# Performance work log

Hardware: AMD Instinct MI355X
Metric: run time of the kernel (lower is better)

The kernel has to match this reference:

```python
import jax, jax.numpy as jnp
import numpy as np

B, T, D, W, H = 8, 2048, 1024, 16, 8
HD = D // H  # head dim = 128
EPS = 1e-5


def _layernorm(x, g, b):
    m = jnp.mean(x, axis=-1, keepdims=True)
    v = jnp.var(x, axis=-1, keepdims=True)
    return (x - m) / jnp.sqrt(v + EPS) * g + b


def setup_inputs() -> dict:
    key = jax.random.key(0)
    ks = jax.random.split(key, 8)
    s = 0.02
    return {
        "frame_features": jax.random.normal(ks[0], (B, T, D), dtype=jnp.float32),
        "frame_indices": jnp.arange(B * T, dtype=jnp.int64).reshape(B, T),
        # nn.MultiheadAttention packed in-projection (3D, D) and out projection
        "w_qkv": jax.random.normal(ks[1], (3 * D, D), dtype=jnp.float32) * s,
        "b_qkv": jnp.zeros((3 * D,), dtype=jnp.float32),
        "w_out": jax.random.normal(ks[2], (D, D), dtype=jnp.float32) * s,
        "b_out": jnp.zeros((D,), dtype=jnp.float32),
        # FFN: Linear(D, 4D) -> GELU -> Linear(4D, D)
        "w1": jax.random.normal(ks[3], (4 * D, D), dtype=jnp.float32) * s,
        "b1": jnp.zeros((4 * D,), dtype=jnp.float32),
        "w2": jax.random.normal(ks[4], (D, 4 * D), dtype=jnp.float32) * s,
        "b2": jnp.zeros((D,), dtype=jnp.float32),
        "g1": jnp.ones((D,), dtype=jnp.float32),
        "beta1": jnp.zeros((D,), dtype=jnp.float32),
        "g2": jnp.ones((D,), dtype=jnp.float32),
        "beta2": jnp.zeros((D,), dtype=jnp.float32),
    }


def _forward(frame_features, frame_indices, w_qkv, b_qkv, w_out, b_out,
             w1, b1, w2, b2, g1, beta1, g2, beta2):
    # --- sinusoidal temporal positional encoding, indexed by frame number ---
    pos = frame_indices.astype(jnp.float32)[..., None]          # (B, T, 1)
    div = jnp.exp(-jnp.log(10000.0) * jnp.arange(0, D, 2, dtype=jnp.float32) / D)
    ang = pos * div                                              # (B, T, D/2)
    pe = jnp.stack([jnp.sin(ang), jnp.cos(ang)], axis=-1).reshape(B, T, D)
    x = frame_features + pe

    # --- block-diagonal (local window) attention, all windows in one pass ---
    nw = T // W
    xw = x.reshape(B, nw, W, D)
    qkv = jnp.einsum('bnwd,ed->bnwe', xw, w_qkv) + b_qkv         # (B, nw, W, 3D)
    q, k, v = jnp.split(qkv, 3, axis=-1)
    q = q.reshape(B, nw, W, H, HD)
    k = k.reshape(B, nw, W, H, HD)
    v = v.reshape(B, nw, W, H, HD)
    scores = jnp.einsum('bnqhd,bnkhd->bnhqk', q, k) / jnp.sqrt(jnp.float32(HD))
    attn = jax.nn.softmax(scores, axis=-1)
    o = jnp.einsum('bnhqk,bnkhd->bnqhd', attn, v).reshape(B, nw, W, D)
    attn_out = jnp.einsum('bnwd,ed->bnwe', o, w_out) + b_out

    h = _layernorm(xw + attn_out, g1, beta1)
    ffn = jnp.einsum('bnwf,df->bnwd', jax.nn.gelu(
        jnp.einsum('bnwd,fd->bnwf', h, w1) + b1, approximate=False), w2) + b2
    out = _layernorm(h + ffn, g2, beta2)
    return out.reshape(B, T, D)


def reference(frame_features, frame_indices, w_qkv, b_qkv, w_out, b_out,
              w1, b1, w2, b2, g1, beta1, g2, beta2):
    return _forward(frame_features, frame_indices, w_qkv, b_qkv, w_out, b_out,
                    w1, b1, w2, b2, g1, beta1, g2, beta2)
```

## Files before the change

### kernel.cpp

```cpp
#include <hip/hip_runtime.h>
#include <math.h>

typedef __bf16 bf16;
typedef __bf16 bf16x8 __attribute__((ext_vector_type(8)));
typedef __bf16 bf16x4 __attribute__((ext_vector_type(4)));
typedef __bf16 bf16x2 __attribute__((ext_vector_type(2)));
typedef float f32x4 __attribute__((ext_vector_type(4)));

#define ROWS 16384

typedef __attribute__((address_space(3))) void* lds_vp;
typedef const __attribute__((address_space(1))) void* glb_vp;
__device__ __forceinline__ void gload16(const void* g, void* l) {
  __builtin_amdgcn_global_load_lds((glb_vp)g, (lds_vp)l, 16, 0, 0);
}

__global__ __launch_bounds__(256) void cast_kernel(
    const float* __restrict__ src, bf16* __restrict__ dst, int n)
{
  int i = (blockIdx.x * 256 + threadIdx.x) * 8;
  if (i >= n) return;
  float4 a = *(const float4*)(src + i);
  float4 b = *(const float4*)(src + i + 4);
  bf16x8 o;
  o[0] = (bf16)a.x; o[1] = (bf16)a.y; o[2] = (bf16)a.z; o[3] = (bf16)a.w;
  o[4] = (bf16)b.x; o[5] = (bf16)b.y; o[6] = (bf16)b.z; o[7] = (bf16)b.w;
  *(bf16x8*)(dst + i) = o;
}

__global__ __launch_bounds__(256) void pe_add_kernel(
    const float* __restrict__ ff, const int* __restrict__ idx, bf16* __restrict__ x)
{
  int p   = blockIdx.x * 256 + threadIdx.x;
  int row = p >> 9;
  int j   = p & 511;
  float pos = (float)idx[row];
  float d2  = (float)(2 * j) * (1.0f / 1024.0f);
  float dv  = expf(-9.210340371976184f * d2);
  float ang = pos * dv;
  float s, c;
  sincosf(ang, &s, &c);
  int base = row * 1024 + 2 * j;
  float2 f = *(const float2*)(ff + base);
  bf16x2 o;
  o[0] = (bf16)(f.x + s);
  o[1] = (bf16)(f.y + c);
  *(bf16x2*)(x + base) = o;
}

#define MFMA16 __builtin_amdgcn_mfma_f32_16x16x32_bf16

template<bool GELU, bool RES>
__global__ __launch_bounds__(512, 2) void gemm8(
    const bf16* __restrict__ A, const bf16* __restrict__ Bw,
    const float* __restrict__ bias, const bf16* __restrict__ resid,
    bf16* __restrict__ C, int M, int N, int K)
{
  extern __shared__ char smem[];
  bf16* lA = (bf16*)smem;
  bf16* lB = (bf16*)(smem + 65536);

  const int tid  = threadIdx.x;
  const int wave = tid >> 6;
  const int lane = tid & 63;
  const int wm = wave >> 2, wn = wave & 3;
  const int ln = lane & 15, q = lane >> 4;
  const int wm8 = wm * 8, wn4 = wn * 4;
  const int rsw = (ln * 32 + q * 8) ^ (((ln >> 3) & 1) << 4);

  const int nwg = gridDim.x;
  const int nbn = N >> 8;
  const int swz = (blockIdx.x & 7) * (nwg >> 3) + (blockIdx.x >> 3);
  const int bm = (swz / nbn) << 8;
  const int bn = (swz % nbn) << 8;

  const int le = lane ^ (((lane >> 5) & 1) << 1);
  const int sr = le >> 2;
  const int sc = (le & 3) * 8;
  const bf16* gA = A  + (size_t)(bm + wave * 16 + sr) * K + sc;
  const bf16* gB = Bw + (size_t)(bn + wave * 16 + sr) * K + sc;
  const size_t hstep = (size_t)128 * K;

#define STAGE_A(h, bb, kk) do { \
    bf16* _d = lA + (bb) * 16384 + ((h) * 8 + wave) * 1024; \
    gload16(gA + (size_t)(h) * hstep + (kk), _d); \
    gload16(gA + (size_t)(h) * hstep + (kk) + 32, _d + 512); } while (0)
#define STAGE_B(h, bb, kk) do { \
    bf16* _d = lB + (bb) * 16384 + ((h) * 8 + wave) * 1024; \
    gload16(gB + (size_t)(h) * hstep + (kk), _d); \
    gload16(gB + (size_t)(h) * hstep + (kk) + 32, _d + 512); } while (0)
#define LDA8(dst, t, ks, bb) (dst) = *(const bf16x8*)(lA + (bb) * 16384 + (wm8 + (t)) * 1024 + (ks) * 512 + rsw)
#define LDB8(dst, n, ks, bb) (dst) = *(const bf16x8*)(lB + (bb) * 16384 + (wn4 + (n)) * 1024 + (ks) * 512 + rsw)

  f32x4 acc[8][4];
#pragma unroll
  for (int i = 0; i < 8; i++)
#pragma unroll
    for (int j = 0; j < 4; j++) acc[i][j] = {0.f, 0.f, 0.f, 0.f};

  const int nkt = K >> 6;

  STAGE_A(0, 0, 0);  STAGE_A(1, 0, 0);
  STAGE_B(0, 0, 0);  STAGE_B(1, 0, 0);
  STAGE_A(0, 1, 64); STAGE_A(1, 1, 64);
  asm volatile("s_waitcnt vmcnt(4)");

  bf16x8 alo[4][2], ahi[4][2], bq[2][2];

  for (int m = 0; m < nkt; ++m) {
    const int b  = m & 1;
    const int k0 = m << 6;

    __builtin_amdgcn_s_barrier();
    if (m + 1 < nkt) STAGE_B(0, b ^ 1, k0 + 64);
#pragma unroll
    for (int t = 0; t < 4; t++) { LDA8(alo[t][0], t, 0, b); LDA8(alo[t][1], t, 1, b); }
    LDB8(bq[0][0], 0, 0, b); LDB8(bq[0][1], 0, 1, b);
    LDB8(bq[1][0], 1, 0, b); LDB8(bq[1][1], 1, 1, b);
    __builtin_amdgcn_s_setprio(1);
#pragma unroll
    for (int t = 0; t < 4; t++)
#pragma unroll
      for (int n = 0; n < 2; n++) {
        acc[t][n] = MFMA16(alo[t][0], bq[n][0], acc[t][n], 0, 0, 0);
        acc[t][n] = MFMA16(alo[t][1], bq[n][1], acc[t][n], 0, 0, 0);
      }
    __builtin_amdgcn_s_setprio(0);

    __builtin_amdgcn_s_barrier();
    if (m + 1 < nkt) STAGE_B(1, b ^ 1, k0 + 64);
#pragma unroll
    for (int t = 0; t < 4; t++) { LDA8(ahi[t][0], t + 4, 0, b); LDA8(ahi[t][1], t + 4, 1, b); }
    __builtin_amdgcn_s_setprio(1);
#pragma unroll
    for (int t = 0; t < 4; t++)
#pragma unroll
      for (int n = 0; n < 2; n++) {
        acc[t + 4][n] = MFMA16(ahi[t][0], bq[n][0], acc[t + 4][n], 0, 0, 0);
        acc[t + 4][n] = MFMA16(ahi[t][1], bq[n][1], acc[t + 4][n], 0, 0, 0);
      }
    __builtin_amdgcn_s_setprio(0);

    __builtin_amdgcn_s_barrier();
    if (m + 2 < nkt) STAGE_A(0, b, k0 + 128);
    LDB8(bq[0][0], 2, 0, b); LDB8(bq[0][1], 2, 1, b);
    LDB8(bq[1][0], 3, 0, b); LDB8(bq[1][1], 3, 1, b);
    __builtin_amdgcn_s_setprio(1);
#pragma unroll
    for (int t = 0; t < 4; t++)
#pragma unroll
      for (int n = 0; n < 2; n++) {
        acc[t][n + 2] = MFMA16(alo[t][0], bq[n][0], acc[t][n + 2], 0, 0, 0);
        acc[t][n + 2] = MFMA16(alo[t][1], bq[n][1], acc[t][n + 2], 0, 0, 0);
      }
    __builtin_amdgcn_s_setprio(0);

    __builtin_amdgcn_s_barrier();
    if (m + 2 < nkt) STAGE_A(1, b, k0 + 128);
    __builtin_amdgcn_s_setprio(1);
#pragma unroll
    for (int t = 0; t < 4; t++)
#pragma unroll
      for (int n = 0; n < 2; n++) {
        acc[t + 4][n + 2] = MFMA16(ahi[t][0], bq[n][0], acc[t + 4][n + 2], 0, 0, 0);
        acc[t + 4][n + 2] = MFMA16(ahi[t][1], bq[n][1], acc[t + 4][n + 2], 0, 0, 0);
      }
    __builtin_amdgcn_s_setprio(0);
    if (m == nkt - 2)     { asm volatile("s_waitcnt vmcnt(0)"); }
    else if (m < nkt - 2) { asm volatile("s_waitcnt vmcnt(4)"); }
  }

  float bv[4];
#pragma unroll
  for (int tn = 0; tn < 4; tn++) bv[tn] = bias[bn + wn * 64 + tn * 16 + ln];
  bf16* eb = (bf16*)smem;
  const int lrow = tid >> 4;
  const int cb   = (tid & 15) * 16;
#pragma unroll
  for (int tm = 0; tm < 8; tm++) {
    __syncthreads();
#pragma unroll
    for (int tn = 0; tn < 4; tn++)
#pragma unroll
      for (int i = 0; i < 4; i++)
        eb[(wm * 16 + q * 4 + i) * 264 + wn * 64 + tn * 16 + ln] =
            (bf16)(acc[tm][tn][i] + bv[tn]);
    __syncthreads();
    int gR = bm + (lrow >> 4) * 128 + tm * 16 + (lrow & 15);
    size_t rowoff = (size_t)gR * N + bn + cb;
    bf16x8 v0 = *(const bf16x8*)&eb[lrow * 264 + cb];
    bf16x8 v1 = *(const bf16x8*)&eb[lrow * 264 + cb + 8];
    if (RES) {
      bf16x8 r0 = *(const bf16x8*)(resid + rowoff);
      bf16x8 r1 = *(const bf16x8*)(resid + rowoff + 8);
#pragma unroll
      for (int u = 0; u < 8; u++) {
        v0[u] = (bf16)((float)v0[u] + (float)r0[u]);
        v1[u] = (bf16)((float)v1[u] + (float)r1[u]);
      }
    }
    if (GELU) {
#pragma unroll
      for (int u = 0; u < 8; u++) {
        float a = (float)v0[u], c = (float)v1[u];
        float ea = __builtin_amdgcn_exp2f(2.3022082f * a * (1.0f + 0.044715f * a * a));
        float ec = __builtin_amdgcn_exp2f(2.3022082f * c * (1.0f + 0.044715f * c * c));
        v0[u] = (bf16)(a - a * __builtin_amdgcn_rcpf(ea + 1.0f));
        v1[u] = (bf16)(c - c * __builtin_amdgcn_rcpf(ec + 1.0f));
      }
    }
    *(bf16x8*)(C + rowoff)     = v0;
    *(bf16x8*)(C + rowoff + 8) = v1;
  }
#undef STAGE_A
#undef STAGE_B
#undef LDA8
#undef LDB8
}

__global__ __launch_bounds__(256) void attn_kernel(
    const bf16* __restrict__ qkv, bf16* __restrict__ o)
{
  __shared__ float sq[16][132], sk[16][132], sv[16][132];
  __shared__ float ss[16][17];

  int wid = blockIdx.x;
  int h   = wid & 7;
  int win = wid >> 3;
  int tb  = win * 16;

  int t  = threadIdx.x;
  int r  = t >> 4;
  int c8 = (t & 15) * 8;

  const bf16* base = qkv + (size_t)(tb + r) * 3072 + c8;
  bf16x8 qv = *(const bf16x8*)(base + h * 128);
  bf16x8 kv = *(const bf16x8*)(base + 1024 + h * 128);
  bf16x8 vv = *(const bf16x8*)(base + 2048 + h * 128);
#pragma unroll
  for (int u = 0; u < 8; u++) {
    sq[r][c8 + u] = (float)qv[u];
    sk[r][c8 + u] = (float)kv[u];
    sv[r][c8 + u] = (float)vv[u];
  }
  __syncthreads();

  {
    int i = t >> 4, jj = t & 15;
    float s = 0.f;
#pragma unroll 8
    for (int d = 0; d < 128; d++) s += sq[i][d] * sk[jj][d];
    ss[i][jj] = s * 0.08838834764831845f;
  }
  __syncthreads();

  if (t < 16) {
    float m = -1e30f;
    for (int jj = 0; jj < 16; jj++) m = fmaxf(m, ss[t][jj]);
    float sum = 0.f;
    for (int jj = 0; jj < 16; jj++) { float e = expf(ss[t][jj] - m); ss[t][jj] = e; sum += e; }
    float inv = 1.0f / sum;
    for (int jj = 0; jj < 16; jj++) ss[t][jj] *= inv;
  }
  __syncthreads();

  {
    int i = t >> 4; int d0 = (t & 15) * 8;
    float acc[8] = {0, 0, 0, 0, 0, 0, 0, 0};
#pragma unroll
    for (int jj = 0; jj < 16; jj++) {
      float a = ss[i][jj];
#pragma unroll
      for (int u = 0; u < 8; u++) acc[u] += a * sv[jj][d0 + u];
    }
    bf16* op = o + (size_t)(tb + i) * 1024 + h * 128 + d0;
#pragma unroll
    for (int u = 0; u < 8; u++) op[u] = (bf16)acc[u];
  }
}

template<typename OUT_T>
__global__ __launch_bounds__(256) void ln_kernel(
    const bf16* __restrict__ x, const float* __restrict__ g,
    const float* __restrict__ b, OUT_T* __restrict__ y)
{
  __shared__ float red[8];
  int row = blockIdx.x;
  int t   = threadIdx.x;
  int lane = t & 63, wave = t >> 6;

  bf16x4 v4 = *(const bf16x4*)(x + (size_t)row * 1024 + t * 4);
  float v[4];
  float s = 0.f, sq = 0.f;
#pragma unroll
  for (int u = 0; u < 4; u++) {
    v[u] = (float)v4[u];
    s += v[u];
    sq += v[u] * v[u];
  }
  for (int off = 32; off > 0; off >>= 1) {
    s  += __shfl_down(s, off);
    sq += __shfl_down(sq, off);
  }
  if (lane == 0) { red[wave * 2] = s; red[wave * 2 + 1] = sq; }
  __syncthreads();
  float st = red[0] + red[2] + red[4] + red[6];
  float qt = red[1] + red[3] + red[5] + red[7];
  float mean = st * (1.0f / 1024.0f);
  float var  = qt * (1.0f / 1024.0f) - mean * mean;
  float inv  = rsqrtf(var + 1e-5f);
  int c = t * 4;
  OUT_T* yr = y + (size_t)row * 1024 + c;
#pragma unroll
  for (int u = 0; u < 4; u++)
    yr[u] = (OUT_T)((v[u] - mean) * inv * g[c + u] + b[c + u]);
}

extern "C" void kernel_launch(void* const* d_in, const int* in_sizes, int n_in,
                              void* d_out, int out_size, void* d_ws, size_t ws_size,
                              hipStream_t stream) {
  const float* ff    = (const float*)d_in[0];
  const int*   idx   = (const int*)d_in[1];
  const float* w_qkv = (const float*)d_in[2];
  const float* b_qkv = (const float*)d_in[3];
  const float* w_out = (const float*)d_in[4];
  const float* b_out = (const float*)d_in[5];
  const float* w1    = (const float*)d_in[6];
  const float* b1    = (const float*)d_in[7];
  const float* w2    = (const float*)d_in[8];
  const float* b2    = (const float*)d_in[9];
  const float* g1    = (const float*)d_in[10];
  const float* be1   = (const float*)d_in[11];
  const float* g2    = (const float*)d_in[12];
  const float* be2   = (const float*)d_in[13];
  float* out = (float*)d_out;

  static bool attrs_done = false;
  if (!attrs_done) {
    attrs_done = true;
    hipFuncSetAttribute(reinterpret_cast<const void*>(&gemm8<false, false>),
                        hipFuncAttributeMaxDynamicSharedMemorySize, 131072);
    hipFuncSetAttribute(reinterpret_cast<const void*>(&gemm8<false, true>),
                        hipFuncAttributeMaxDynamicSharedMemorySize, 131072);
    hipFuncSetAttribute(reinterpret_cast<const void*>(&gemm8<true, false>),
                        hipFuncAttributeMaxDynamicSharedMemorySize, 131072);
  }

  char* p = (char*)d_ws;
  bf16* x_bf = (bf16*)p;  p += (size_t)ROWS * 1024 * 2;
  bf16* big  = (bf16*)p;  p += (size_t)ROWS * 4096 * 2;
  bf16* s_bf = (bf16*)p;  p += (size_t)ROWS * 1024 * 2;
  bf16* h_bf = (bf16*)p;  p += (size_t)ROWS * 1024 * 2;
  bf16* wqb  = (bf16*)p;  p += (size_t)3072 * 1024 * 2;
  bf16* wob  = (bf16*)p;  p += (size_t)1024 * 1024 * 2;
  bf16* w1b  = (bf16*)p;  p += (size_t)4096 * 1024 * 2;
  bf16* w2b  = (bf16*)p;  p += (size_t)1024 * 4096 * 2;
  bf16* o_bf = big + (size_t)ROWS * 3072;
  bf16* g_bf = big;

  cast_kernel<<<3072 * 1024 / 8 / 256, 256, 0, stream>>>(w_qkv, wqb, 3072 * 1024);
  cast_kernel<<<1024 * 1024 / 8 / 256, 256, 0, stream>>>(w_out, wob, 1024 * 1024);
  cast_kernel<<<4096 * 1024 / 8 / 256, 256, 0, stream>>>(w1, w1b, 4096 * 1024);
  cast_kernel<<<1024 * 4096 / 8 / 256, 256, 0, stream>>>(w2, w2b, 1024 * 4096);

  pe_add_kernel<<<ROWS * 512 / 256, 256, 0, stream>>>(ff, idx, x_bf);

  gemm8<false, false><<<64 * 12, 512, 131072, stream>>>(
      x_bf, wqb, b_qkv, nullptr, big, ROWS, 3072, 1024);
  attn_kernel<<<(ROWS / 16) * 8, 256, 0, stream>>>(big, o_bf);
  gemm8<false, true><<<64 * 4, 512, 131072, stream>>>(
      o_bf, wob, b_out, x_bf, s_bf, ROWS, 1024, 1024);
  ln_kernel<bf16><<<ROWS, 256, 0, stream>>>(s_bf, g1, be1, h_bf);
  gemm8<true, false><<<64 * 16, 512, 131072, stream>>>(
      h_bf, w1b, b1, nullptr, big, ROWS, 4096, 1024);
  gemm8<false, true><<<64 * 4, 512, 131072, stream>>>(
      g_bf, w2b, b2, h_bf, s_bf, ROWS, 1024, 4096);
  ln_kernel<float><<<ROWS, 256, 0, stream>>>(s_bf, g2, be2, out);
}
```

Measured before the change: 664.0 us.

## Rework GEMM mainloop into 4-stage K=32 pipeline with inline ds_read offsets

The bf16 GEMM main loop now uses K-steps of 32 with a four-buffer ring in LDS instead of a double-buffered K=64 scheme. Global-to-LDS loads are issued three stages ahead. LDS fragment reads use inline-asm ds_read_b128 with immediate offsets, and sched_barrier plus explicit lgkmcnt waits fence each MFMA burst. The goal is deeper prefetch to hide global latency and lower address-arithmetic overhead. The costs are more barriers per unit of K and a loop that assumes nkt is a multiple of 4 with a carefully tuned vmcnt sequence.

```diff
diff --git a/kernel.cpp b/kernel.cpp
--- a/kernel.cpp
+++ b/kernel.cpp
@@ -11,8 +11,16 @@
 
 typedef __attribute__((address_space(3))) void* lds_vp;
 typedef const __attribute__((address_space(1))) void* glb_vp;
+typedef __attribute__((address_space(3))) bf16 lbf16;
 __device__ __forceinline__ void gload16(const void* g, void* l) {
   __builtin_amdgcn_global_load_lds((glb_vp)g, (lds_vp)l, 16, 0, 0);
+}
+
+template<int OFF>
+__device__ __forceinline__ bf16x8 dsr(uint32_t a) {
+  bf16x8 r;
+  asm volatile("ds_read_b128 %0, %1 offset:%2" : "=v"(r) : "v"(a), "n"(OFF));
+  return r;
 }
 
 __global__ __launch_bounds__(256) void cast_kernel(
@@ -57,8 +65,6 @@
     bf16* __restrict__ C, int M, int N, int K)
 {
   extern __shared__ char smem[];
-  bf16* lA = (bf16*)smem;
-  bf16* lB = (bf16*)(smem + 65536);
 
   const int tid  = threadIdx.x;
   const int wave = tid >> 6;
@@ -66,7 +72,6 @@
   const int wm = wave >> 2, wn = wave & 3;
   const int ln = lane & 15, q = lane >> 4;
   const int wm8 = wm * 8, wn4 = wn * 4;
-  const int rsw = (ln * 32 + q * 8) ^ (((ln >> 3) & 1) << 4);
 
   const int nwg = gridDim.x;
   const int nbn = N >> 8;
@@ -74,23 +79,27 @@
   const int bm = (swz / nbn) << 8;
   const int bn = (swz % nbn) << 8;
 
+  const uint32_t lbase = (uint32_t)(size_t)(lbf16*)smem;
+  const uint32_t rswb  = (uint32_t)((ln * 64 + q * 16) ^ (((ln >> 3) & 1) << 5));
+  const uint32_t rA01 = lbase + wm8 * 1024 + rswb;
+  const uint32_t rA23 = rA01 + 65536;
+  const uint32_t rB01 = lbase + 16384 + wn4 * 1024 + rswb;
+  const uint32_t rB23 = rB01 + 65536;
+
   const int le = lane ^ (((lane >> 5) & 1) << 1);
   const int sr = le >> 2;
   const int sc = (le & 3) * 8;
-  const bf16* gA = A  + (size_t)(bm + wave * 16 + sr) * K + sc;
-  const bf16* gB = Bw + (size_t)(bn + wave * 16 + sr) * K + sc;
-  const size_t hstep = (size_t)128 * K;
-
-#define STAGE_A(h, bb, kk) do { \
-    bf16* _d = lA + (bb) * 16384 + ((h) * 8 + wave) * 1024; \
-    gload16(gA + (size_t)(h) * hstep + (kk), _d); \
-    gload16(gA + (size_t)(h) * hstep + (kk) + 32, _d + 512); } while (0)
-#define STAGE_B(h, bb, kk) do { \
-    bf16* _d = lB + (bb) * 16384 + ((h) * 8 + wave) * 1024; \
-    gload16(gB + (size_t)(h) * hstep + (kk), _d); \
-    gload16(gB + (size_t)(h) * hstep + (kk) + 32, _d + 512); } while (0)
-#define LDA8(dst, t, ks, bb) (dst) = *(const bf16x8*)(lA + (bb) * 16384 + (wm8 + (t)) * 1024 + (ks) * 512 + rsw)
-#define LDB8(dst, n, ks, bb) (dst) = *(const bf16x8*)(lB + (bb) * 16384 + (wn4 + (n)) * 1024 + (ks) * 512 + rsw)
+  const bf16* gAw = A  + (size_t)(bm + wave * 32 + sr) * K + sc;
+  const bf16* gBw = Bw + (size_t)(bn + wave * 32 + sr) * K + sc;
+
+#define STAGE_A(BB, KOFF) do { \
+    char* _d = smem + (BB) * 32768 + wave * 2048; \
+    gload16(gAw + (KOFF), _d); \
+    gload16(gAw + 16 * (size_t)K + (KOFF), _d + 1024); } while (0)
+#define STAGE_B(BB, KOFF) do { \
+    char* _d = smem + (BB) * 32768 + 16384 + wave * 2048; \
+    gload16(gBw + (KOFF), _d); \
+    gload16(gBw + 16 * (size_t)K + (KOFF), _d + 1024); } while (0)
 
   f32x4 acc[8][4];
 #pragma unroll
@@ -98,77 +107,73 @@
 #pragma unroll
     for (int j = 0; j < 4; j++) acc[i][j] = {0.f, 0.f, 0.f, 0.f};
 
-  const int nkt = K >> 6;
-
-  STAGE_A(0, 0, 0);  STAGE_A(1, 0, 0);
-  STAGE_B(0, 0, 0);  STAGE_B(1, 0, 0);
-  STAGE_A(0, 1, 64); STAGE_A(1, 1, 64);
-  asm volatile("s_waitcnt vmcnt(4)");
-
-  bf16x8 alo[4][2], ahi[4][2], bq[2][2];
-
-  for (int m = 0; m < nkt; ++m) {
-    const int b  = m & 1;
-    const int k0 = m << 6;
-
-    __builtin_amdgcn_s_barrier();
-    if (m + 1 < nkt) STAGE_B(0, b ^ 1, k0 + 64);
-#pragma unroll
-    for (int t = 0; t < 4; t++) { LDA8(alo[t][0], t, 0, b); LDA8(alo[t][1], t, 1, b); }
-    LDB8(bq[0][0], 0, 0, b); LDB8(bq[0][1], 0, 1, b);
-    LDB8(bq[1][0], 1, 0, b); LDB8(bq[1][1], 1, 1, b);
-    __builtin_amdgcn_s_setprio(1);
-#pragma unroll
-    for (int t = 0; t < 4; t++)
-#pragma unroll
-      for (int n = 0; n < 2; n++) {
-        acc[t][n] = MFMA16(alo[t][0], bq[n][0], acc[t][n], 0, 0, 0);
-        acc[t][n] = MFMA16(alo[t][1], bq[n][1], acc[t][n], 0, 0, 0);
-      }
-    __builtin_amdgcn_s_setprio(0);
-
-    __builtin_amdgcn_s_barrier();
-    if (m + 1 < nkt) STAGE_B(1, b ^ 1, k0 + 64);
-#pragma unroll
-    for (int t = 0; t < 4; t++) { LDA8(ahi[t][0], t + 4, 0, b); LDA8(ahi[t][1], t + 4, 1, b); }
-    __builtin_amdgcn_s_setprio(1);
-#pragma unroll
-    for (int t = 0; t < 4; t++)
-#pragma unroll
-      for (int n = 0; n < 2; n++) {
-        acc[t + 4][n] = MFMA16(ahi[t][0], bq[n][0], acc[t + 4][n], 0, 0, 0);
-        acc[t + 4][n] = MFMA16(ahi[t][1], bq[n][1], acc[t + 4][n], 0, 0, 0);
-      }
-    __builtin_amdgcn_s_setprio(0);
-
-    __builtin_amdgcn_s_barrier();
-    if (m + 2 < nkt) STAGE_A(0, b, k0 + 128);
-    LDB8(bq[0][0], 2, 0, b); LDB8(bq[0][1], 2, 1, b);
-    LDB8(bq[1][0], 3, 0, b); LDB8(bq[1][1], 3, 1, b);
-    __builtin_amdgcn_s_setprio(1);
-#pragma unroll
-    for (int t = 0; t < 4; t++)
-#pragma unroll
-      for (int n = 0; n < 2; n++) {
-        acc[t][n + 2] = MFMA16(alo[t][0], bq[n][0], acc[t][n + 2], 0, 0, 0);
-        acc[t][n + 2] = MFMA16(alo[t][1], bq[n][1], acc[t][n + 2], 0, 0, 0);
-      }
-    __builtin_amdgcn_s_setprio(0);
-
-    __builtin_amdgcn_s_barrier();
-    if (m + 2 < nkt) STAGE_A(1, b, k0 + 128);
-    __builtin_amdgcn_s_setprio(1);
-#pragma unroll
-    for (int t = 0; t < 4; t++)
-#pragma unroll
-      for (int n = 0; n < 2; n++) {
-        acc[t + 4][n + 2] = MFMA16(ahi[t][0], bq[n][0], acc[t + 4][n + 2], 0, 0, 0);
-        acc[t + 4][n + 2] = MFMA16(ahi[t][1], bq[n][1], acc[t + 4][n + 2], 0, 0, 0);
-      }
-    __builtin_amdgcn_s_setprio(0);
-    if (m == nkt - 2)     { asm volatile("s_waitcnt vmcnt(0)"); }
-    else if (m < nkt - 2) { asm volatile("s_waitcnt vmcnt(4)"); }
-  }
+  const int nkt = K >> 5;
+
+  STAGE_A(0, 0);  STAGE_B(0, 0);
+  STAGE_A(1, 32); STAGE_B(1, 32);
+  STAGE_A(2, 64); STAGE_B(2, 64);
+  asm volatile("s_waitcnt vmcnt(8)");
+  __builtin_amdgcn_s_barrier();
+
+  bf16x8 a0, a1, a2, a3, a4, a5, a6, a7, b0, b1, b2, b3;
+
+#define MF4(T, AT) \
+    acc[T][0] = MFMA16(AT, b0, acc[T][0], 0, 0, 0); \
+    acc[T][1] = MFMA16(AT, b1, acc[T][1], 0, 0, 0); \
+    acc[T][2] = MFMA16(AT, b2, acc[T][2], 0, 0, 0); \
+    acc[T][3] = MFMA16(AT, b3, acc[T][3], 0, 0, 0);
+
+#define PH1(BB, M) { \
+    const uint32_t _ra = (BB) < 2 ? rA01 : rA23; \
+    const uint32_t _rb = (BB) < 2 ? rB01 : rB23; \
+    a0 = dsr<(((BB) & 1) * 32768) + 0>(_ra); \
+    a1 = dsr<(((BB) & 1) * 32768) + 1024>(_ra); \
+    a2 = dsr<(((BB) & 1) * 32768) + 2048>(_ra); \
+    a3 = dsr<(((BB) & 1) * 32768) + 3072>(_ra); \
+    b0 = dsr<(((BB) & 1) * 32768) + 0>(_rb); \
+    b1 = dsr<(((BB) & 1) * 32768) + 1024>(_rb); \
+    b2 = dsr<(((BB) & 1) * 32768) + 2048>(_rb); \
+    b3 = dsr<(((BB) & 1) * 32768) + 3072>(_rb); \
+    if ((M) + 3 < nkt) STAGE_A((((BB) + 3) & 3), ((M) + 3) * 32); \
+    __builtin_amdgcn_s_barrier(); \
+    asm volatile("s_waitcnt lgkmcnt(0)"); \
+    __builtin_amdgcn_sched_barrier(0); \
+    __builtin_amdgcn_s_setprio(1); \
+    MF4(0, a0) MF4(1, a1) MF4(2, a2) MF4(3, a3) \
+    __builtin_amdgcn_s_setprio(0); \
+    __builtin_amdgcn_sched_barrier(0); \
+  }
+
+#define PH2(BB, M) { \
+    const uint32_t _ra = (BB) < 2 ? rA01 : rA23; \
+    a4 = dsr<(((BB) & 1) * 32768) + 4096>(_ra); \
+    a5 = dsr<(((BB) & 1) * 32768) + 5120>(_ra); \
+    a6 = dsr<(((BB) & 1) * 32768) + 6144>(_ra); \
+    a7 = dsr<(((BB) & 1) * 32768) + 7168>(_ra); \
+    if ((M) + 3 < nkt) STAGE_B((((BB) + 3) & 3), ((M) + 3) * 32); \
+    asm volatile("s_waitcnt lgkmcnt(0)"); \
+    __builtin_amdgcn_sched_barrier(0); \
+    __builtin_amdgcn_s_setprio(1); \
+    MF4(4, a4) MF4(5, a5) MF4(6, a6) MF4(7, a7) \
+    __builtin_amdgcn_s_setprio(0); \
+    __builtin_amdgcn_sched_barrier(0); \
+    if ((M) < nkt - 3)       { asm volatile("s_waitcnt vmcnt(8)"); } \
+    else if ((M) == nkt - 3) { asm volatile("s_waitcnt vmcnt(4)"); } \
+    else if ((M) == nkt - 2) { asm volatile("s_waitcnt vmcnt(0)"); } \
+    __builtin_amdgcn_s_barrier(); \
+  }
+
+  for (int mm = 0; mm < nkt; mm += 4) {
+    PH1(0, mm)     PH2(0, mm)
+    PH1(1, mm + 1) PH2(1, mm + 1)
+    PH1(2, mm + 2) PH2(2, mm + 2)
+    PH1(3, mm + 3) PH2(3, mm + 3)
+  }
+#undef PH1
+#undef PH2
+#undef MF4
+#undef STAGE_A
+#undef STAGE_B
 
   float bv[4];
 #pragma unroll
@@ -212,10 +217,6 @@
     *(bf16x8*)(C + rowoff)     = v0;
     *(bf16x8*)(C + rowoff + 8) = v1;
   }
-#undef STAGE_A
-#undef STAGE_B
-#undef LDA8
-#undef LDB8
 }
 
 __global__ __launch_bounds__(256) void attn_kernel(
```

Result: no change. 676.8 us (+1.9%).
